# Performance work log

Hardware: AMD Instinct MI355X
Metric: run time of the kernel (lower is better)

The kernel has to match this reference:

```python
import jax, jax.numpy as jnp
import numpy as np

EPS = 1e-6
LN_EPS = 1e-5  # torch.nn.LayerNorm default


def setup_inputs() -> dict:
    key = jax.random.key(0)
    k1, k2, k3, k4 = jax.random.split(key, 4)
    B, T, L, S, C = 32, 512, 5, 9, 64
    x = jax.random.normal(k1, (B, T), dtype=jnp.float32)
    ws = jax.random.uniform(k2, (S, C), dtype=jnp.float32, minval=-1.0, maxval=1.0)
    bs = jax.random.uniform(k3, (S, C), dtype=jnp.float32, minval=-1.0, maxval=1.0)
    loc_emb = 0.02 * jax.random.normal(k4, (L, C), dtype=jnp.float32)
    # scales = base_bias**i for i in -(S-1)//2 .. (S+1)//2 - 1  (base_bias=10, S=9 -> 10^-4..10^4)
    scales = jnp.asarray([10.0 ** i for i in range(-(S - 1) // 2, (S + 1) // 2)], dtype=jnp.float32)
    locs = jnp.asarray([-2.0, -1.0, 0.0, 1.0, 2.0], dtype=jnp.float32)
    return {"x": x, "ws": ws, "bs": bs, "loc_emb": loc_emb, "scales": scales, "locs": locs}


def reference(x, ws, bs, loc_emb, scales, locs):
    # x: (B, T); locs: (L,); scales: (S,); ws/bs: (S, C); loc_emb: (L, C)
    loc_dis = x[..., None] - locs                                  # (B, T, L)
    # location weights
    loc_w = 1.0 / (jnp.log(jnp.abs(loc_dis) + 1.0) + EPS)          # (B, T, L)
    loc_w = loc_w / jnp.sum(loc_w, axis=-1, keepdims=True)
    # scale weights
    scale_w = 1.0 / (jnp.abs(jnp.log(jnp.abs(loc_dis)[..., None] / scales + EPS)) + EPS)  # (B, T, L, S)
    scale_w = scale_w / jnp.sum(scale_w, axis=-1, keepdims=True)
    # broadcast encode: (B, T, L, 1, 1) * (S, C) + (S, C) * (S, 1) -> (B, T, L, S, C)
    enc = loc_dis[..., None, None] * ws + bs * scales[:, None]
    # LayerNorm over channel dim, no affine
    mean = jnp.mean(enc, axis=-1, keepdims=True)
    var = jnp.mean(jnp.square(enc - mean), axis=-1, keepdims=True)
    enc = (enc - mean) * jax.lax.rsqrt(var + LN_EPS)
    # weighted sum over scales -> (B, T, L, C)
    enc = jnp.sum(enc * scale_w[..., None], axis=-2)
    enc = enc + loc_emb
    # weighted sum over locations -> (B, T, C)
    enc = jnp.sum(enc * loc_w[..., None], axis=-2)
    return enc


if __name__ == "__main__":
    out = reference(**setup_inputs())
    print(out.shape, out.dtype)
```

## Files before the change

kernel.cpp:

```cpp
#include <hip/hip_runtime.h>
#include <math.h>


#define EPS_W 1e-6f
#define LN_EPS 1e-5f
#define LOG_EPS -13.815511f

constexpr int L = 5;
constexpr int S = 9;
constexpr int C = 64;
constexpr int PW = 16;
constexpr int POS = 64;

__device__ __forceinline__ float fastrcp(float v) { return __builtin_amdgcn_rcpf(v); }

__global__ __launch_bounds__(256) void mbe4_kernel(
    const float* __restrict__ x,
    const float* __restrict__ ws,
    const float* __restrict__ bs,
    const float* __restrict__ loc_emb,
    const float* __restrict__ scales,
    const float* __restrict__ locs,
    float* __restrict__ out,
    int npos)
{
    const int tid = threadIdx.x;
    const int lane = tid & 63;
    const int wid = tid >> 6;

    __shared__ float4 statsLds[S][2];
    __shared__ float4 coefLds[POS][6];

    const int pbase = blockIdx.x * POS + wid * PW;

    float xv = 0.0f;
    const int myp = pbase + lane;
    if (lane < PW && myp < npos) xv = x[myp];

    float w[S], k[S], le[L];
#pragma unroll
    for (int s = 0; s < S; ++s) {
        w[s] = ws[s * C + lane];
        k[s] = bs[s * C + lane] * scales[s];
    }
#pragma unroll
    for (int l = 0; l < L; ++l) le[l] = loc_emb[l * C + lane];

    for (int s = wid; s < S; s += 4) {
        float a0 = w[s], a1 = k[s];
        float a2 = w[s] * w[s], a3 = w[s] * k[s], a4 = k[s] * k[s];
#pragma unroll
        for (int off = 32; off; off >>= 1) {
            a0 += __shfl_xor(a0, off);
            a1 += __shfl_xor(a1, off);
            a2 += __shfl_xor(a2, off);
            a3 += __shfl_xor(a3, off);
            a4 += __shfl_xor(a4, off);
        }
        if (lane == 0) {
            float mww = a0 * (1.0f / 64.0f);
            float mkk = a1 * (1.0f / 64.0f);
            statsLds[s][0] = make_float4(
                mww, mkk,
                fmaf(-mww, mww, a2 * (1.0f / 64.0f)),
                2.0f * fmaf(-mww, mkk, a3 * (1.0f / 64.0f)));
            statsLds[s][1] = make_float4(
                fmaf(-mkk, mkk, a4 * (1.0f / 64.0f)),
                __logf(scales[s]), 0.0f, 0.0f);
        }
    }
    __syncthreads();

    if (lane < PW && myp < npos) {
        float mw[S], mk[S], vw[S], c2[S], vk[S], lg[S];
#pragma unroll
        for (int s = 0; s < S; ++s) {
            float4 a = statsLds[s][0];
            float4 b = statsLds[s][1];
            mw[s] = a.x; mk[s] = a.y; vw[s] = a.z; c2[s] = a.w;
            vk[s] = b.x; lg[s] = b.y;
        }

        float d[L], lwv[L], llog[L];
        float lwsum = 0.0f;
#pragma unroll
        for (int l = 0; l < L; ++l) {
            d[l] = xv - locs[l];
            float ad = fabsf(d[l]);
            lwv[l] = fastrcp(__logf(ad + 1.0f) + EPS_W);
            lwsum += lwv[l];
            llog[l] = __logf(ad);
        }
        const float rlw = fastrcp(lwsum);

        float cf[24];
#pragma unroll
        for (int j = 0; j < 24; ++j) cf[j] = 0.0f;

#pragma unroll
        for (int l = 0; l < L; ++l) {
            const float dd = d[l];
            const float d2 = dd * dd;
            const float lwn = lwv[l] * rlw;
            cf[18 + l] = lwn;

            float swv[S];
            float ssum = 0.0f;
#pragma unroll
            for (int s = 0; s < S; ++s) {
                float u = fmaxf(llog[l] - lg[s], LOG_EPS);
                swv[s] = fastrcp(fabsf(u) + EPS_W);
                ssum += swv[s];
            }
            const float rss = fastrcp(ssum) * lwn;

#pragma unroll
            for (int s = 0; s < S; ++s) {
                float mean = fmaf(dd, mw[s], mk[s]);
                float var = fmaf(d2, vw[s], fmaf(dd, c2[s], vk[s]));
                float rstd = rsqrtf(var + LN_EPS);
                float alpha = swv[s] * rss * rstd;
                cf[s] = fmaf(alpha, dd, cf[s]);
                cf[9 + s] += alpha;
                cf[23] = fmaf(-alpha, mean, cf[23]);
            }
        }

        const int row = wid * PW + lane;
#pragma unroll
        for (int j = 0; j < 6; ++j)
            coefLds[row][j] = make_float4(cf[4 * j], cf[4 * j + 1],
                                          cf[4 * j + 2], cf[4 * j + 3]);
    }

#pragma unroll
    for (int i = 0; i < PW; ++i) {
        const int p = pbase + i;
        if (p >= npos) break;
        const int row = wid * PW + i;
        float4 q0 = coefLds[row][0];
        float4 q1 = coefLds[row][1];
        float4 q2 = coefLds[row][2];
        float4 q3 = coefLds[row][3];
        float4 q4 = coefLds[row][4];
        float4 q5 = coefLds[row][5];
        float acc = q5.w;
        acc = fmaf(q0.x, w[0], acc); acc = fmaf(q0.y, w[1], acc);
        acc = fmaf(q0.z, w[2], acc); acc = fmaf(q0.w, w[3], acc);
        acc = fmaf(q1.x, w[4], acc); acc = fmaf(q1.y, w[5], acc);
        acc = fmaf(q1.z, w[6], acc); acc = fmaf(q1.w, w[7], acc);
        acc = fmaf(q2.x, w[8], acc);
        acc = fmaf(q2.y, k[0], acc); acc = fmaf(q2.z, k[1], acc);
        acc = fmaf(q2.w, k[2], acc); acc = fmaf(q3.x, k[3], acc);
        acc = fmaf(q3.y, k[4], acc); acc = fmaf(q3.z, k[5], acc);
        acc = fmaf(q3.w, k[6], acc); acc = fmaf(q4.x, k[7], acc);
        acc = fmaf(q4.y, k[8], acc);
        acc = fmaf(q4.z, le[0], acc); acc = fmaf(q4.w, le[1], acc);
        acc = fmaf(q5.x, le[2], acc); acc = fmaf(q5.y, le[3], acc);
        acc = fmaf(q5.z, le[4], acc);
        out[(size_t)p * C + lane] = acc;
    }
}

extern "C" void kernel_launch(void* const* d_in, const int* in_sizes, int n_in,
                              void* d_out, int out_size, void* d_ws, size_t ws_size,
                              hipStream_t stream) {
    const float* x = (const float*)d_in[0];
    const float* ws = (const float*)d_in[1];
    const float* bs = (const float*)d_in[2];
    const float* loc_emb = (const float*)d_in[3];
    const float* scales = (const float*)d_in[4];
    const float* locs = (const float*)d_in[5];
    float* out = (float*)d_out;

    int npos = in_sizes[0];
    int blocks = (npos + POS - 1) / POS;
    mbe4_kernel<<<blocks, 256, 0, stream>>>(x, ws, bs, loc_emb, scales, locs, out, npos);
}
```

Measured before the change: 12.63 us.

## Split per-position coefficient work across lanes, one location per lane

Each position's coefficient computation is now spread over 8 lanes, one per location, with only 5 of the 8 doing work. Per-lane partial coefficients are combined with xor-shuffle reductions. Positions per wave and per block are halved, which doubles the grid to spread the serial log/rcp/rsqrt chain across more lanes. In exchange it adds 72 shuffles per thread and wastes 3 of every 8 lanes, and each block now writes fewer rows of output.

```diff
diff --git a/kernel.cpp b/kernel.cpp
--- a/kernel.cpp
+++ b/kernel.cpp
@@ -9,12 +9,12 @@
 constexpr int L = 5;
 constexpr int S = 9;
 constexpr int C = 64;
-constexpr int PW = 16;
-constexpr int POS = 64;
+constexpr int PW = 8;
+constexpr int POS = 32;
 
 __device__ __forceinline__ float fastrcp(float v) { return __builtin_amdgcn_rcpf(v); }
 
-__global__ __launch_bounds__(256) void mbe4_kernel(
+__global__ __launch_bounds__(256) void mbe5_kernel(
     const float* __restrict__ x,
     const float* __restrict__ ws,
     const float* __restrict__ bs,
@@ -32,10 +32,12 @@
     __shared__ float4 coefLds[POS][6];
 
     const int pbase = blockIdx.x * POS + wid * PW;
+    const int q = lane & 7;
+    const int gi = lane >> 3;
+    const int p = pbase + gi;
 
-    float xv = 0.0f;
-    const int myp = pbase + lane;
-    if (lane < PW && myp < npos) xv = x[myp];
+    const int pc = p < npos ? p : (npos - 1);
+    const float xv = x[pc];
 
     float w[S], k[S], le[L];
 #pragma unroll
@@ -71,62 +73,63 @@
     }
     __syncthreads();
 
-    if (lane < PW && myp < npos) {
-        float mw[S], mk[S], vw[S], c2[S], vk[S], lg[S];
+    float cf[24];
+#pragma unroll
+    for (int j = 0; j < 24; ++j) cf[j] = 0.0f;
+
+    float lwv = 0.0f, llog_ = 0.0f, dl = 0.0f;
+    const bool act = (q < L) && (p < npos);
+    if (act) {
+        dl = xv - locs[q];
+        float ad = fabsf(dl);
+        lwv = fastrcp(__logf(ad + 1.0f) + EPS_W);
+        llog_ = __logf(ad);
+    }
+    float lwsum = lwv;
+    lwsum += __shfl_xor(lwsum, 1);
+    lwsum += __shfl_xor(lwsum, 2);
+    lwsum += __shfl_xor(lwsum, 4);
+    const float lwn = lwv * fastrcp(lwsum);
+    cf[18] = (q == 0) ? lwn : 0.0f;
+    cf[19] = (q == 1) ? lwn : 0.0f;
+    cf[20] = (q == 2) ? lwn : 0.0f;
+    cf[21] = (q == 3) ? lwn : 0.0f;
+    cf[22] = (q == 4) ? lwn : 0.0f;
+
+    if (act) {
+        float swv[S];
+        float ssum = 0.0f;
+#pragma unroll
+        for (int s = 0; s < S; ++s) {
+            float lg = statsLds[s][1].y;
+            float u = fmaxf(llog_ - lg, LOG_EPS);
+            swv[s] = fastrcp(fabsf(u) + EPS_W);
+            ssum += swv[s];
+        }
+        const float rss = fastrcp(ssum) * lwn;
+        const float d2 = dl * dl;
 #pragma unroll
         for (int s = 0; s < S; ++s) {
             float4 a = statsLds[s][0];
             float4 b = statsLds[s][1];
-            mw[s] = a.x; mk[s] = a.y; vw[s] = a.z; c2[s] = a.w;
-            vk[s] = b.x; lg[s] = b.y;
+            float mean = fmaf(dl, a.x, a.y);
+            float var = fmaf(d2, a.z, fmaf(dl, a.w, b.x));
+            float rstd = rsqrtf(var + LN_EPS);
+            float alpha = swv[s] * rss * rstd;
+            cf[s] = alpha * dl;
+            cf[9 + s] = alpha;
+            cf[23] = fmaf(-alpha, mean, cf[23]);
         }
-
-        float d[L], lwv[L], llog[L];
-        float lwsum = 0.0f;
-#pragma unroll
-        for (int l = 0; l < L; ++l) {
-            d[l] = xv - locs[l];
-            float ad = fabsf(d[l]);
-            lwv[l] = fastrcp(__logf(ad + 1.0f) + EPS_W);
-            lwsum += lwv[l];
-            llog[l] = __logf(ad);
-        }
-        const float rlw = fastrcp(lwsum);
-
-        float cf[24];
-#pragma unroll
-        for (int j = 0; j < 24; ++j) cf[j] = 0.0f;
+    }
 
 #pragma unroll
-        for (int l = 0; l < L; ++l) {
-            const float dd = d[l];
-            const float d2 = dd * dd;
-            const float lwn = lwv[l] * rlw;
-            cf[18 + l] = lwn;
+    for (int off = 1; off <= 4; off <<= 1) {
+#pragma unroll
+        for (int j = 0; j < 24; ++j) cf[j] += __shfl_xor(cf[j], off);
+    }
 
-            float swv[S];
-            float ssum = 0.0f;
-#pragma unroll
-            for (int s = 0; s < S; ++s) {
-                float u = fmaxf(llog[l] - lg[s], LOG_EPS);
-                swv[s] = fastrcp(fabsf(u) + EPS_W);
-                ssum += swv[s];
-            }
-            const float rss = fastrcp(ssum) * lwn;
-
-#pragma unroll
-            for (int s = 0; s < S; ++s) {
-                float mean = fmaf(dd, mw[s], mk[s]);
-                float var = fmaf(d2, vw[s], fmaf(dd, c2[s], vk[s]));
-                float rstd = rsqrtf(var + LN_EPS);
-                float alpha = swv[s] * rss * rstd;
-                cf[s] = fmaf(alpha, dd, cf[s]);
-                cf[9 + s] += alpha;
-                cf[23] = fmaf(-alpha, mean, cf[23]);
-            }
-        }
-
-        const int row = wid * PW + lane;
+    if (q == 0 && p < npos) {
+        const int row = wid * PW + gi;
 #pragma unroll
         for (int j = 0; j < 6; ++j)
             coefLds[row][j] = make_float4(cf[4 * j], cf[4 * j + 1],
@@ -135,8 +138,8 @@
 
 #pragma unroll
     for (int i = 0; i < PW; ++i) {
-        const int p = pbase + i;
-        if (p >= npos) break;
+        const int pp = pbase + i;
+        if (pp >= npos) break;
         const int row = wid * PW + i;
         float4 q0 = coefLds[row][0];
         float4 q1 = coefLds[row][1];
@@ -158,7 +161,7 @@
         acc = fmaf(q4.z, le[0], acc); acc = fmaf(q4.w, le[1], acc);
         acc = fmaf(q5.x, le[2], acc); acc = fmaf(q5.y, le[3], acc);
         acc = fmaf(q5.z, le[4], acc);
-        out[(size_t)p * C + lane] = acc;
+        out[(size_t)pp * C + lane] = acc;
     }
 }
 
@@ -175,5 +178,5 @@
 
     int npos = in_sizes[0];
     int blocks = (npos + POS - 1) / POS;
-    mbe4_kernel<<<blocks, 256, 0, stream>>>(x, ws, bs, loc_emb, scales, locs, out, npos);
+    mbe5_kernel<<<blocks, 256, 0, stream>>>(x, ws, bs, loc_emb, scales, locs, out, npos);
 }
```

New measurement: 13.31 us. 5.4% more time.

## Split per-position scale computation across four lanes with shuffle reductions

Applied to the files above, without the earlier changes.

Assigns four lanes per position instead of one, each handling a subset of the nine scales, and reduces the scale-weight sums and the constant term with cross-lane shuffles. This uses all 64 lanes in the coefficient phase instead of only 16, shortening the serial rsqrt/rcp chain per lane. It adds shuffles, scattered scalar LDS writes and redundant log work per lane.

```diff
diff --git a/kernel.cpp b/kernel.cpp
--- a/kernel.cpp
+++ b/kernel.cpp
@@ -14,7 +14,7 @@
 
 __device__ __forceinline__ float fastrcp(float v) { return __builtin_amdgcn_rcpf(v); }
 
-__global__ __launch_bounds__(256) void mbe4_kernel(
+__global__ __launch_bounds__(256) void mbe6_kernel(
     const float* __restrict__ x,
     const float* __restrict__ ws,
     const float* __restrict__ bs,
@@ -29,13 +29,15 @@
     const int wid = tid >> 6;
 
     __shared__ float4 statsLds[S][2];
-    __shared__ float4 coefLds[POS][6];
-
+    __shared__ alignas(16) float coefLds[POS][24];
+
+    const int gi = lane >> 2;
+    const int q = lane & 3;
     const int pbase = blockIdx.x * POS + wid * PW;
-
-    float xv = 0.0f;
-    const int myp = pbase + lane;
-    if (lane < PW && myp < npos) xv = x[myp];
+    const int p = pbase + gi;
+
+    const int pc = p < npos ? p : (npos - 1);
+    const float xv = x[pc];
 
     float w[S], k[S], le[L];
 #pragma unroll
@@ -71,79 +73,107 @@
     }
     __syncthreads();
 
-    if (lane < PW && myp < npos) {
-        float mw[S], mk[S], vw[S], c2[S], vk[S], lg[S];
-#pragma unroll
-        for (int s = 0; s < S; ++s) {
+    float d_[L], llog_[L], lwv_[L];
+    float lwsum = 0.0f;
+#pragma unroll
+    for (int l = 0; l < L; ++l) {
+        d_[l] = xv - locs[l];
+        float ad = fabsf(d_[l]);
+        lwv_[l] = fastrcp(__logf(ad + 1.0f) + EPS_W);
+        lwsum += lwv_[l];
+        llog_[l] = __logf(ad);
+    }
+    const float rlw = fastrcp(lwsum);
+
+    float mwj[3], mkj[3], vwj[3], c2j[3], vkj[3], lgj[3];
+#pragma unroll
+    for (int j = 0; j < 3; ++j) {
+        int s = q + 4 * j;
+        if (s < S) {
             float4 a = statsLds[s][0];
             float4 b = statsLds[s][1];
-            mw[s] = a.x; mk[s] = a.y; vw[s] = a.z; c2[s] = a.w;
-            vk[s] = b.x; lg[s] = b.y;
-        }
-
-        float d[L], lwv[L], llog[L];
-        float lwsum = 0.0f;
-#pragma unroll
-        for (int l = 0; l < L; ++l) {
-            d[l] = xv - locs[l];
-            float ad = fabsf(d[l]);
-            lwv[l] = fastrcp(__logf(ad + 1.0f) + EPS_W);
-            lwsum += lwv[l];
-            llog[l] = __logf(ad);
-        }
-        const float rlw = fastrcp(lwsum);
-
-        float cf[24];
-#pragma unroll
-        for (int j = 0; j < 24; ++j) cf[j] = 0.0f;
-
-#pragma unroll
-        for (int l = 0; l < L; ++l) {
-            const float dd = d[l];
-            const float d2 = dd * dd;
-            const float lwn = lwv[l] * rlw;
-            cf[18 + l] = lwn;
-
-            float swv[S];
-            float ssum = 0.0f;
-#pragma unroll
-            for (int s = 0; s < S; ++s) {
-                float u = fmaxf(llog[l] - lg[s], LOG_EPS);
-                swv[s] = fastrcp(fabsf(u) + EPS_W);
-                ssum += swv[s];
+            mwj[j] = a.x; mkj[j] = a.y; vwj[j] = a.z; c2j[j] = a.w;
+            vkj[j] = b.x; lgj[j] = b.y;
+        } else {
+            mwj[j] = mkj[j] = vwj[j] = c2j[j] = lgj[j] = 0.0f;
+            vkj[j] = 1.0f;
+        }
+    }
+
+    float swv[3][L];
+    float pss[L];
+#pragma unroll
+    for (int l = 0; l < L; ++l) {
+        float t = 0.0f;
+#pragma unroll
+        for (int j = 0; j < 3; ++j) {
+            int s = q + 4 * j;
+            float u = fmaxf(llog_[l] - lgj[j], LOG_EPS);
+            float v = fastrcp(fabsf(u) + EPS_W);
+            v = (s < S) ? v : 0.0f;
+            swv[j][l] = v;
+            t += v;
+        }
+        pss[l] = t;
+    }
+#pragma unroll
+    for (int l = 0; l < L; ++l) {
+        pss[l] += __shfl_xor(pss[l], 1);
+        pss[l] += __shfl_xor(pss[l], 2);
+    }
+
+    float Aj[3] = {0.0f, 0.0f, 0.0f};
+    float Bj[3] = {0.0f, 0.0f, 0.0f};
+    float cnst = 0.0f;
+#pragma unroll
+    for (int l = 0; l < L; ++l) {
+        const float lwn = lwv_[l] * rlw;
+        const float rss = fastrcp(pss[l]) * lwn;
+        const float dd = d_[l];
+        const float d2 = dd * dd;
+#pragma unroll
+        for (int j = 0; j < 3; ++j) {
+            float mean = fmaf(dd, mwj[j], mkj[j]);
+            float var = fmaf(d2, vwj[j], fmaf(dd, c2j[j], vkj[j]));
+            float rstd = rsqrtf(var + LN_EPS);
+            float alpha = swv[j][l] * rss * rstd;
+            Aj[j] = fmaf(alpha, dd, Aj[j]);
+            Bj[j] += alpha;
+            cnst = fmaf(-alpha, mean, cnst);
+        }
+    }
+    cnst += __shfl_xor(cnst, 1);
+    cnst += __shfl_xor(cnst, 2);
+
+    if (p < npos) {
+        const int row = wid * PW + gi;
+#pragma unroll
+        for (int j = 0; j < 3; ++j) {
+            int s = q + 4 * j;
+            if (s < S) {
+                coefLds[row][s] = Aj[j];
+                coefLds[row][9 + s] = Bj[j];
             }
-            const float rss = fastrcp(ssum) * lwn;
-
-#pragma unroll
-            for (int s = 0; s < S; ++s) {
-                float mean = fmaf(dd, mw[s], mk[s]);
-                float var = fmaf(d2, vw[s], fmaf(dd, c2[s], vk[s]));
-                float rstd = rsqrtf(var + LN_EPS);
-                float alpha = swv[s] * rss * rstd;
-                cf[s] = fmaf(alpha, dd, cf[s]);
-                cf[9 + s] += alpha;
-                cf[23] = fmaf(-alpha, mean, cf[23]);
-            }
-        }
-
-        const int row = wid * PW + lane;
-#pragma unroll
-        for (int j = 0; j < 6; ++j)
-            coefLds[row][j] = make_float4(cf[4 * j], cf[4 * j + 1],
-                                          cf[4 * j + 2], cf[4 * j + 3]);
+        }
+        if (q == 0) {
+#pragma unroll
+            for (int l = 0; l < L; ++l) coefLds[row][18 + l] = lwv_[l] * rlw;
+            coefLds[row][23] = cnst;
+        }
     }
 
 #pragma unroll
     for (int i = 0; i < PW; ++i) {
-        const int p = pbase + i;
-        if (p >= npos) break;
+        const int pp = pbase + i;
+        if (pp >= npos) break;
         const int row = wid * PW + i;
-        float4 q0 = coefLds[row][0];
-        float4 q1 = coefLds[row][1];
-        float4 q2 = coefLds[row][2];
-        float4 q3 = coefLds[row][3];
-        float4 q4 = coefLds[row][4];
-        float4 q5 = coefLds[row][5];
+        const float4* cr = (const float4*)coefLds[row];
+        float4 q0 = cr[0];
+        float4 q1 = cr[1];
+        float4 q2 = cr[2];
+        float4 q3 = cr[3];
+        float4 q4 = cr[4];
+        float4 q5 = cr[5];
         float acc = q5.w;
         acc = fmaf(q0.x, w[0], acc); acc = fmaf(q0.y, w[1], acc);
         acc = fmaf(q0.z, w[2], acc); acc = fmaf(q0.w, w[3], acc);
@@ -158,7 +188,7 @@
         acc = fmaf(q4.z, le[0], acc); acc = fmaf(q4.w, le[1], acc);
         acc = fmaf(q5.x, le[2], acc); acc = fmaf(q5.y, le[3], acc);
         acc = fmaf(q5.z, le[4], acc);
-        out[(size_t)p * C + lane] = acc;
+        out[(size_t)pp * C + lane] = acc;
     }
 }
 
@@ -175,5 +205,5 @@
 
     int npos = in_sizes[0];
     int blocks = (npos + POS - 1) / POS;
-    mbe4_kernel<<<blocks, 256, 0, stream>>>(x, ws, bs, loc_emb, scales, locs, out, npos);
+    mbe6_kernel<<<blocks, 256, 0, stream>>>(x, ws, bs, loc_emb, scales, locs, out, npos);
 }
```

Result: no change. 12.61 us (-0.1%).
